# Kernel tuning notes

Measured on AMD Instinct MI355X. Metric: run time of the kernel, lower is better.

## Reference

```python
import jax, jax.numpy as jnp
import numpy as np
import math

DIM = 512


def setup_inputs() -> dict:
    key = jax.random.key(0)
    ks = jax.random.split(key, 6)
    B, N, D = 4, 4096, DIM
    H = D // 2
    features = jax.random.normal(ks[0], (B, N, D), dtype=jnp.float32)
    W1 = jax.random.normal(ks[1], (D, H), dtype=jnp.float32) * 0.02
    b1 = jnp.zeros((H,), dtype=jnp.float32)
    ln_g = jnp.ones((H,), dtype=jnp.float32)
    ln_b = jnp.zeros((H,), dtype=jnp.float32)
    W2 = jax.random.normal(ks[2], (H, 1), dtype=jnp.float32) * 0.02
    b2 = jnp.zeros((1,), dtype=jnp.float32)
    target_entropy = jnp.ones((1,), dtype=jnp.float32) * math.log(D)
    temperature = jnp.ones((1,), dtype=jnp.float32)
    return {"features": features, "W1": W1, "b1": b1, "ln_g": ln_g,
            "ln_b": ln_b, "W2": W2, "b2": b2,
            "target_entropy": target_entropy, "temperature": temperature}


def _layernorm(x, g, b, eps=1e-5):
    mu = jnp.mean(x, axis=-1, keepdims=True)
    var = jnp.mean((x - mu) ** 2, axis=-1, keepdims=True)
    return (x - mu) * jax.lax.rsqrt(var + eps) * g + b


def reference(features, W1, b1, ln_g, ln_b, W2, b2, target_entropy, temperature):
    # ---- compute_entropy: pairwise RBF kernel over [B, N, D] ----
    sq = jnp.sum(features ** 2, axis=-1)                       # [B, N]
    gram = jnp.einsum('bnd,bmd->bnm', features, features)      # [B, N, N]
    d2 = jnp.maximum(sq[:, :, None] + sq[:, None, :] - 2.0 * gram, 0.0)
    tau = temperature[0]
    kernel = jnp.exp(-d2 / (2.0 * tau ** 2))                   # [B, N, N]
    probs = kernel / jnp.sum(kernel, axis=-1, keepdims=True)
    entropy = -jnp.sum(probs * jnp.log(probs + 1e-6), axis=-1)  # [B, N]

    # ---- entropy estimator MLP (computed in original forward, output unused) ----
    h = features @ W1 + b1
    h = _layernorm(h, ln_g, ln_b)
    h = jax.nn.gelu(h, approximate=False)
    estimated_entropy = h @ W2 + b2                            # [B, N, 1] (unused)
    del estimated_entropy

    # ---- sigmoid-gated control signal ----
    entropy_diff = entropy - target_entropy[0]
    control_signal = jax.nn.sigmoid(-entropy_diff / tau)       # [B, N]
    controlled_features = features * control_signal[..., None]
    return controlled_features, control_signal
```

## Files before the change

### kernel.cpp

```cpp
#include <hip/hip_runtime.h>
#include <stdint.h>

#define N_TOK 4096
#define DIM   512
#define BATCH 4
#define BN    (BATCH * N_TOK)
#define JSPLIT 8
#define IPW   64
#define IPB   256
#define NG    (N_TOK / JSPLIT / 16)

typedef __attribute__((ext_vector_type(4))) float f32x4;
typedef __attribute__((ext_vector_type(8))) int   i32x8;

typedef const __attribute__((address_space(1))) uint32_t* gptr_t;
typedef __attribute__((address_space(3))) uint32_t* lptr_t;

__device__ __forceinline__ float sumsq8(uint lo, uint hi) {
    float s = 0.f, f;
    f = __builtin_amdgcn_cvt_f32_fp8((int)lo, 0); s = fmaf(f, f, s);
    f = __builtin_amdgcn_cvt_f32_fp8((int)lo, 1); s = fmaf(f, f, s);
    f = __builtin_amdgcn_cvt_f32_fp8((int)lo, 2); s = fmaf(f, f, s);
    f = __builtin_amdgcn_cvt_f32_fp8((int)lo, 3); s = fmaf(f, f, s);
    f = __builtin_amdgcn_cvt_f32_fp8((int)hi, 0); s = fmaf(f, f, s);
    f = __builtin_amdgcn_cvt_f32_fp8((int)hi, 1); s = fmaf(f, f, s);
    f = __builtin_amdgcn_cvt_f32_fp8((int)hi, 2); s = fmaf(f, f, s);
    f = __builtin_amdgcn_cvt_f32_fp8((int)hi, 3); s = fmaf(f, f, s);
    return s;
}

__global__ __launch_bounds__(256) void prep_kernel(
    const float* __restrict__ feat, uint8_t* __restrict__ fb,
    uint8_t* __restrict__ fbT, float* __restrict__ sq)
{
    __shared__ __align__(16) long lt[1024];
    const int t = threadIdx.x;
    const int row16 = t >> 4, seg = t & 15;
    const size_t grp = blockIdx.x;
    const size_t row = grp * 16 + row16;

    const float4* src = (const float4*)(feat + row * DIM + seg * 32);
    uint32_t wd[8];
    float s = 0.f;
#pragma unroll
    for (int i = 0; i < 4; ++i) {
        float4 a = src[2 * i], b = src[2 * i + 1];
        uint lo = (uint)__builtin_amdgcn_cvt_pk_fp8_f32(a.x, a.y, 0, false);
        lo      = (uint)__builtin_amdgcn_cvt_pk_fp8_f32(a.z, a.w, (int)lo, true);
        uint hi = (uint)__builtin_amdgcn_cvt_pk_fp8_f32(b.x, b.y, 0, false);
        hi      = (uint)__builtin_amdgcn_cvt_pk_fp8_f32(b.z, b.w, (int)hi, true);
        wd[2 * i] = lo; wd[2 * i + 1] = hi;
        s += sumsq8(lo, hi);
    }

    uint4* dst = (uint4*)(fb + row * DIM + seg * 32);
    uint4 o0; o0.x = wd[0]; o0.y = wd[1]; o0.z = wd[2]; o0.w = wd[3];
    uint4 o1; o1.x = wd[4]; o1.y = wd[5]; o1.z = wd[6]; o1.w = wd[7];
    dst[0] = o0; dst[1] = o1;

#pragma unroll
    for (int i = 0; i < 4; ++i) {
        int c = seg * 4 + i;
        long d = ((long)(unsigned)wd[2 * i + 1] << 32) | (unsigned)wd[2 * i];
        lt[c * 16 + ((row16 + c) & 15)] = d;
    }

#pragma unroll
    for (int m = 1; m < 16; m <<= 1) s += __shfl_xor(s, m);
    if (seg == 0) sq[row] = s;

    __syncthreads();
    long* ot = (long*)(fbT + grp * 8192);
#pragma unroll
    for (int i = 0; i < 4; ++i) {
        int p    = t + i * 256;
        int kk   = p >> 8;
        int rem  = p & 255;
        int half = rem >> 7;
        int l6   = (rem >> 1) & 63;
        int qq   = l6 >> 4;
        int r    = l6 & 15;
        int w8   = half * 2 + (p & 1);
        int c    = kk * 16 + qq * 4 + w8;
        ot[p] = lt[c * 16 + ((r + c) & 15)];
    }
}

__global__ __launch_bounds__(256, 2) void entropy_kernel(
    const uint8_t* __restrict__ fb, const uint8_t* __restrict__ fbT,
    const float* __restrict__ sq, const float* __restrict__ temp,
    float* __restrict__ Sp, float* __restrict__ Tp)
{
    __shared__ uint4 Bs[2][512];
    const int t    = threadIdx.x;
    const int w    = t >> 6;
    const int lane = t & 63;
    const int q    = lane >> 4;
    const int c16  = lane & 15;
    const int lbo  = lane * 16;

    const int flat  = blockIdx.x;
    const int combo = flat & 31;
    const int batch = combo >> 3;
    const int jh    = combo & 7;
    const int iblk  = flat >> 5;
    const int iw    = iblk * IPB + w * IPW;
    const size_t rowbase = (size_t)batch * N_TOK;

    const float tau    = temp[0];
    const float inv2t2 = 0.5f / (tau * tau);
    const float cg     = 1.0f / (tau * tau);

    i32x8 afrag[4][4];
#pragma unroll
    for (int s = 0; s < 4; ++s) {
        const uint4* ap = (const uint4*)(fb + (rowbase + iw + s * 16 + c16) * DIM);
#pragma unroll
        for (int kk = 0; kk < 4; ++kk) {
            uint4 lo = ap[kk * 8 + q * 2];
            uint4 hi = ap[kk * 8 + q * 2 + 1];
            i32x8 v = {(int)lo.x, (int)lo.y, (int)lo.z, (int)lo.w,
                       (int)hi.x, (int)hi.y, (int)hi.z, (int)hi.w};
            afrag[s][kk] = v;
        }
    }
    float pi[4][4];
#pragma unroll
    for (int s = 0; s < 4; ++s)
#pragma unroll
        for (int r = 0; r < 4; ++r)
            pi[s][r] = -sq[rowbase + iw + s * 16 + q * 4 + r] * inv2t2;

    float S[4][4], T[4][4];
#pragma unroll
    for (int s = 0; s < 4; ++s)
#pragma unroll
        for (int r = 0; r < 4; ++r) { S[s][r] = 0.f; T[s][r] = 0.f; }

    const uint8_t* bgbase = fbT
        + ((size_t)batch * (N_TOK / 16) + (size_t)jh * NG) * 8192;
    const float* sqj = sq + rowbase + jh * (N_TOK / JSPLIT) + c16;

    {
        const uint8_t* gs = bgbase + w * 2048 + lbo;
        uint8_t* ld = (uint8_t*)Bs[0] + w * 2048;
        __builtin_amdgcn_global_load_lds((gptr_t)(const void*)gs,
                                         (lptr_t)(void*)ld, 16, 0, 0);
        __builtin_amdgcn_global_load_lds((gptr_t)(const void*)(gs + 1024),
                                         (lptr_t)(void*)(ld + 1024), 16, 0, 0);
    }
    __syncthreads();

    int cur = 0;
    for (int g = 0; g < NG; ++g) {
        if (g + 1 < NG) {
            const uint8_t* gs = bgbase + (size_t)(g + 1) * 8192 + w * 2048 + lbo;
            uint8_t* ld = (uint8_t*)Bs[cur ^ 1] + w * 2048;
            __builtin_amdgcn_global_load_lds((gptr_t)(const void*)gs,
                                             (lptr_t)(void*)ld, 16, 0, 0);
            __builtin_amdgcn_global_load_lds((gptr_t)(const void*)(gs + 1024),
                                             (lptr_t)(void*)(ld + 1024), 16, 0, 0);
        }
        float pj = -sqj[(size_t)g * 16] * inv2t2;
        const uint8_t* bs = (const uint8_t*)Bs[cur];
        f32x4 acc[4] = {{0,0,0,0},{0,0,0,0},{0,0,0,0},{0,0,0,0}};
#pragma unroll
        for (int kk = 0; kk < 4; ++kk) {
            uint4 lo = *(const uint4*)(bs + kk * 2048 + lbo);
            uint4 hi = *(const uint4*)(bs + kk * 2048 + 1024 + lbo);
            i32x8 b = {(int)lo.x, (int)lo.y, (int)lo.z, (int)lo.w,
                       (int)hi.x, (int)hi.y, (int)hi.z, (int)hi.w};
            acc[0] = __builtin_amdgcn_mfma_scale_f32_16x16x128_f8f6f4(afrag[0][kk], b, acc[0], 0, 0, 0, 127, 0, 127);
            acc[1] = __builtin_amdgcn_mfma_scale_f32_16x16x128_f8f6f4(afrag[1][kk], b, acc[1], 0, 0, 0, 127, 0, 127);
            acc[2] = __builtin_amdgcn_mfma_scale_f32_16x16x128_f8f6f4(afrag[2][kk], b, acc[2], 0, 0, 0, 127, 0, 127);
            acc[3] = __builtin_amdgcn_mfma_scale_f32_16x16x128_f8f6f4(afrag[3][kk], b, acc[3], 0, 0, 0, 127, 0, 127);
        }
        float m = -1e30f;
#pragma unroll
        for (int s = 0; s < 4; ++s)
#pragma unroll
            for (int r = 0; r < 4; ++r) {
                acc[s][r] = fmaf(acc[s][r], cg, pi[s][r] + pj);
                m = fmaxf(m, acc[s][r]);
            }
        if (m > -110.0f) {
#pragma unroll
            for (int s = 0; s < 4; ++s)
#pragma unroll
                for (int r = 0; r < 4; ++r) {
                    float ee = fminf(acc[s][r], 0.f);
                    float k  = __expf(ee);
                    S[s][r] += k;
                    T[s][r]  = fmaf(k, ee, T[s][r]);
                }
        }
        __syncthreads();
        cur ^= 1;
    }

#pragma unroll
    for (int m = 1; m < 16; m <<= 1)
#pragma unroll
        for (int s = 0; s < 4; ++s)
#pragma unroll
            for (int r = 0; r < 4; ++r) {
                S[s][r] += __shfl_xor(S[s][r], m);
                T[s][r] += __shfl_xor(T[s][r], m);
            }

    if (c16 == 0) {
#pragma unroll
        for (int s = 0; s < 4; ++s)
#pragma unroll
            for (int r = 0; r < 4; ++r) {
                size_t idx = (size_t)jh * BN + rowbase + iw + s * 16 + q * 4 + r;
                Sp[idx] = S[s][r];
                Tp[idx] = T[s][r];
            }
    }
}

__global__ __launch_bounds__(256) void finalize_kernel(
    const float* __restrict__ feat, const float* __restrict__ Sp,
    const float* __restrict__ Tp, const float* __restrict__ tgt,
    const float* __restrict__ temp, float* __restrict__ out)
{
    int row  = (blockIdx.x << 2) + (threadIdx.x >> 6);
    int lane = threadIdx.x & 63;
    float S = 0.0f, T = 0.0f;
#pragma unroll
    for (int j = 0; j < JSPLIT; ++j) {
        S += Sp[(size_t)j * BN + row];
        T += Tp[(size_t)j * BN + row];
    }
    float tau = temp[0];
    float E  = __logf(S) - T / S;
    float cs = 1.0f / (1.0f + __expf((E - tgt[0]) / tau));

    const float4* F4 = (const float4*)(feat + (size_t)row * DIM);
    float4*       O4 = (float4*)(out + (size_t)row * DIM);
    float4 v0 = F4[lane], v1 = F4[lane + 64];
    v0.x *= cs; v0.y *= cs; v0.z *= cs; v0.w *= cs;
    v1.x *= cs; v1.y *= cs; v1.z *= cs; v1.w *= cs;
    O4[lane] = v0; O4[lane + 64] = v1;
    if (lane == 0) out[(size_t)BN * DIM + row] = cs;
}

extern "C" void kernel_launch(void* const* d_in, const int* in_sizes, int n_in,
                              void* d_out, int out_size, void* d_ws, size_t ws_size,
                              hipStream_t stream) {
    const float* feat = (const float*)d_in[0];
    const float* tgt  = (const float*)d_in[7];
    const float* temp = (const float*)d_in[8];
    float* out = (float*)d_out;

    char* ws = (char*)d_ws;
    uint8_t* fb  = (uint8_t*)ws;
    uint8_t* fbT = fb + (size_t)BN * DIM;
    float*   sq  = (float*)(fbT + (size_t)BN * DIM);
    float*   Sp  = sq + BN;
    float*   Tp  = Sp + (size_t)JSPLIT * BN;

    prep_kernel<<<dim3(BN / 16), dim3(256), 0, stream>>>(feat, fb, fbT, sq);
    entropy_kernel<<<dim3((N_TOK / IPB) * BATCH * JSPLIT), dim3(256), 0, stream>>>(fb, fbT, sq, temp, Sp, Tp);
    finalize_kernel<<<dim3(BN / 4), dim3(256), 0, stream>>>(feat, Sp, Tp, tgt, temp, out);
}
```

Measured before the change: 150.0 us.

## Deepen LDS B-tile pipeline to 4 buffers, prefetch 2 ahead, preload sq

Replaces the double-buffered B-tile staging with a four-slot ring that prefetches two groups ahead. Each iteration now uses explicit vmcnt waits and a single raw s_barrier instead of the trailing __syncthreads. The per-group sq values are staged once into LDS instead of being read from global memory every iteration, and MFMA issue is wrapped in s_setprio. This aims to hide global-to-LDS latency and cut barrier overhead, at the cost of extra LDS use and fragile hand-written waitcnt and barrier ordering. The sqlds writes have no barrier before first use and rely on the loop's s_barrier, which looks sufficient.

```diff
diff --git a/kernel.cpp b/kernel.cpp
--- a/kernel.cpp
+++ b/kernel.cpp
@@ -91,7 +91,8 @@
     const float* __restrict__ sq, const float* __restrict__ temp,
     float* __restrict__ Sp, float* __restrict__ Tp)
 {
-    __shared__ uint4 Bs[2][512];
+    __shared__ uint4 Bs[4][512];
+    __shared__ float sqlds[NG * 16];
     const int t    = threadIdx.x;
     const int w    = t >> 6;
     const int lane = t & 63;
@@ -131,6 +132,12 @@
         for (int r = 0; r < 4; ++r)
             pi[s][r] = -sq[rowbase + iw + s * 16 + q * 4 + r] * inv2t2;
 
+    {
+        const float* sqslice = sq + rowbase + (size_t)jh * (N_TOK / JSPLIT);
+        sqlds[t]       = sqslice[t];
+        sqlds[t + 256] = sqslice[t + 256];
+    }
+
     float S[4][4], T[4][4];
 #pragma unroll
     for (int s = 0; s < 4; ++s)
@@ -139,31 +146,31 @@
 
     const uint8_t* bgbase = fbT
         + ((size_t)batch * (N_TOK / 16) + (size_t)jh * NG) * 8192;
-    const float* sqj = sq + rowbase + jh * (N_TOK / JSPLIT) + c16;
-
-    {
-        const uint8_t* gs = bgbase + w * 2048 + lbo;
-        uint8_t* ld = (uint8_t*)Bs[0] + w * 2048;
+
+    auto stage = [&](int g) {
+        const uint8_t* gs = bgbase + (size_t)g * 8192 + w * 2048 + lbo;
+        uint8_t* ld = (uint8_t*)(&Bs[g & 3][0]) + w * 2048;
         __builtin_amdgcn_global_load_lds((gptr_t)(const void*)gs,
                                          (lptr_t)(void*)ld, 16, 0, 0);
         __builtin_amdgcn_global_load_lds((gptr_t)(const void*)(gs + 1024),
                                          (lptr_t)(void*)(ld + 1024), 16, 0, 0);
-    }
-    __syncthreads();
-
-    int cur = 0;
+    };
+    stage(0);
+    stage(1);
+    asm volatile("s_waitcnt lgkmcnt(0)" ::: "memory");
+
     for (int g = 0; g < NG; ++g) {
-        if (g + 1 < NG) {
-            const uint8_t* gs = bgbase + (size_t)(g + 1) * 8192 + w * 2048 + lbo;
-            uint8_t* ld = (uint8_t*)Bs[cur ^ 1] + w * 2048;
-            __builtin_amdgcn_global_load_lds((gptr_t)(const void*)gs,
-                                             (lptr_t)(void*)ld, 16, 0, 0);
-            __builtin_amdgcn_global_load_lds((gptr_t)(const void*)(gs + 1024),
-                                             (lptr_t)(void*)(ld + 1024), 16, 0, 0);
-        }
-        float pj = -sqj[(size_t)g * 16] * inv2t2;
-        const uint8_t* bs = (const uint8_t*)Bs[cur];
+        if (g + 2 < NG) stage(g + 2);
+        if (g + 2 < NG)      asm volatile("s_waitcnt vmcnt(4)" ::: "memory");
+        else if (g + 1 < NG) asm volatile("s_waitcnt vmcnt(2)" ::: "memory");
+        else                 asm volatile("s_waitcnt vmcnt(0)" ::: "memory");
+        __builtin_amdgcn_s_barrier();
+        __builtin_amdgcn_sched_barrier(0);
+
+        const uint8_t* bs = (const uint8_t*)(&Bs[g & 3][0]);
+        float pj = -sqlds[g * 16 + c16] * inv2t2;
         f32x4 acc[4] = {{0,0,0,0},{0,0,0,0},{0,0,0,0},{0,0,0,0}};
+        __builtin_amdgcn_s_setprio(1);
 #pragma unroll
         for (int kk = 0; kk < 4; ++kk) {
             uint4 lo = *(const uint4*)(bs + kk * 2048 + lbo);
@@ -175,6 +182,7 @@
             acc[2] = __builtin_amdgcn_mfma_scale_f32_16x16x128_f8f6f4(afrag[2][kk], b, acc[2], 0, 0, 0, 127, 0, 127);
             acc[3] = __builtin_amdgcn_mfma_scale_f32_16x16x128_f8f6f4(afrag[3][kk], b, acc[3], 0, 0, 0, 127, 0, 127);
         }
+        __builtin_amdgcn_s_setprio(0);
         float m = -1e30f;
 #pragma unroll
         for (int s = 0; s < 4; ++s)
@@ -194,8 +202,6 @@
                     T[s][r]  = fmaf(k, ee, T[s][r]);
                 }
         }
-        __syncthreads();
-        cur ^= 1;
     }
 
 #pragma unroll
```

After: 148.4 us. About the same (-1.1%).
